# Kernel optimization log

Hardware: AMD Instinct MI355X
Metric: run time of the kernel (lower is better)

The kernel has to match this reference:

```python
import jax, jax.numpy as jnp
import numpy as np

NA = 3            # n_agents
B = 32768         # batch
H = 128           # hidden_dim (= attend_dim, attend_heads = 1)
ES, OAS, GS, ADIM = 4, 4, 2, 2
SDIM = ES + OAS * (NA - 1) + GS * NA   # 18
EPS = 1e-5


def _bn(x, ax):
    # BatchNorm1d(affine=False) in training mode: normalize with batch stats (biased var)
    m = x.mean(ax, keepdims=True)
    v = x.var(ax, keepdims=True)
    return (x - m) / jnp.sqrt(v + EPS)


def _lrelu(x):
    return jax.nn.leaky_relu(x, 0.01)


def setup_inputs() -> dict:
    key = jax.random.key(0)
    ks = jax.random.split(key, 26)
    r = lambda k, shp: (jax.random.normal(k, shp, dtype=jnp.float32) * 0.05)
    inp = {
        "s": jax.random.normal(ks[0], (NA, B, SDIM), dtype=jnp.float32),
        "a": jax.random.uniform(ks[1], (NA, B, ADIM), dtype=jnp.float32),
        # Attention_Actor (sa_encoder, with_action=True) params
        "en_W": r(ks[2], (NA, ES + 2, H)), "en_b": r(ks[3], (NA, H)),
        "oa_W": r(ks[4], (NA, OAS, H)), "oa_b": r(ks[5], (NA, H)),
        "goal_W": r(ks[6], (NA, GS, H)), "goal_b": r(ks[7], (NA, H)),
        "akey_W": r(ks[8], (2, H, H)),
        "asel_W": r(ks[9], (2, H, H)),
        "aval_W": r(ks[10], (2, H, H)), "aval_b": r(ks[11], (2, H)),
        "merge_W": r(ks[12], (NA, 3 * H, H)), "merge_b": r(ks[13], (NA, H)),
        # Critic params
        "senc_W": r(ks[14], (NA, SDIM, H)), "senc_b": r(ks[15], (NA, H)),
        "ckey_W": r(ks[16], (1, H, H)),
        "csel_W": r(ks[17], (1, H, H)),
        "cval_W": r(ks[18], (1, H, H)), "cval_b": r(ks[19], (1, H)),
        "cW1": r(ks[20], (NA, 2 * H, H)), "cb1": r(ks[21], (NA, H)),
        "cW2": r(ks[22], (NA, H, ADIM)), "cb2": r(ks[23], (NA, ADIM)),
    }
    return inp


def reference(s, a, en_W, en_b, oa_W, oa_b, goal_W, goal_b, akey_W, asel_W,
              aval_W, aval_b, merge_W, merge_b, senc_W, senc_b, ckey_W,
              csel_W, cval_W, cval_b, cW1, cb1, cW2, cb2):
    scale = 1.0 / np.sqrt(H)
    # ---- Attention_Actor(with_action=True): state-action encodings ----
    ent_in = _bn(jnp.concatenate([s[..., :ES], a[..., :2]], -1), 1)           # [NA,B,6]
    en_enc = _lrelu(jnp.einsum('nbi,nih->nbh', ent_in, en_W) + en_b[:, None])  # [NA,B,H]
    # other-agent slices (each slice normalized separately, as separate BN calls)
    oa_in = s[..., ES:ES + OAS * (NA - 1)].reshape(NA, B, NA - 1, OAS).transpose(0, 2, 1, 3)
    oa_enc = _lrelu(jnp.einsum('njbi,nih->njbh', _bn(oa_in, 2), oa_W) + oa_b[:, None, None])
    g_in = s[..., ES + OAS * (NA - 1):].reshape(NA, B, NA, GS).transpose(0, 2, 1, 3)
    g_enc = _lrelu(jnp.einsum('njbi,nih->njbh', _bn(g_in, 2), goal_W) + goal_b[:, None, None])
    sel = jnp.einsum('nbh,mhd->mnbd', en_enc, asel_W)                          # [2,NA,B,H]

    def attend(enc, kW, vW, vb, selm):
        keys = jnp.einsum('njbh,hd->njbd', enc, kW)
        vals = _lrelu(jnp.einsum('njbh,hd->njbd', enc, vW) + vb)
        w = jax.nn.softmax(jnp.einsum('nbd,njbd->nbj', selm, keys) * scale, -1)
        return jnp.einsum('nbj,njbd->nbd', w, vals)

    ov0 = attend(oa_enc, akey_W[0], aval_W[0], aval_b[0], sel[0])
    ov1 = attend(g_enc, akey_W[1], aval_W[1], aval_b[1], sel[1])
    sa_enc = _lrelu(jnp.einsum('nbi,nih->nbh',
                               jnp.concatenate([en_enc, ov0, ov1], -1), merge_W)
                    + merge_b[:, None])                                        # [NA,B,H]
    # ---- Critic: state encoders + cross-agent attention over sa encodings ----
    s_enc = _lrelu(jnp.einsum('nbi,nih->nbh', _bn(s, 1), senc_W) + senc_b[:, None])
    keys = jnp.einsum('nbh,khd->knbd', sa_enc, ckey_W)                         # [1,NA,B,H]
    vals = _lrelu(jnp.einsum('nbh,khd->knbd', sa_enc, cval_W) + cval_b[:, None, None])
    sels = jnp.einsum('nbh,khd->knbd', s_enc, csel_W)
    logits = jnp.einsum('kibd,kjbd->kibj', sels, keys) * scale                 # [1,NA,B,NA]
    mask = jnp.eye(NA, dtype=bool)[None, :, None, :]
    w = jax.nn.softmax(jnp.where(mask, -1e9, logits), -1)                      # attend j != i
    ov = jnp.einsum('kibj,kjbd->kibd', w, vals)                                # [1,NA,B,H]
    ov = jnp.moveaxis(ov, 0, -2).reshape(NA, B, -1)                            # concat heads
    h = _lrelu(jnp.einsum('nbi,nih->nbh', jnp.concatenate([s_enc, ov], -1), cW1)
               + cb1[:, None])
    q = jnp.einsum('nbh,nho->nbo', h, cW2) + cb2[:, None]                      # [NA,B,ADIM]
    return q
```

## Files before the change

kernel.cpp:

```cpp
#include <hip/hip_runtime.h>
#include <hip/hip_bf16.h>

#define NAG 3
#define BATCH 32768
#define HD 128
#define SD 18
#define TB 32
#define ROWS 48
#define NBLK 683
#define PADB (NBLK * ROWS)
#define EPSV 1e-5f
#define SCALE 0.08838834764831845f

typedef __attribute__((ext_vector_type(8))) short short8;
typedef __attribute__((ext_vector_type(4))) float f32x4;

#define WSB_STATS 0
#define WSB_ACCUM 512
#define WSB_F     1024
#define WSB_W     197632
#define OFF_FT0 0
#define OFF_FT1 32768
#define OFF_MT  65536
#define OFF_AV0 98304
#define OFF_AV1 131072
#define OFF_CV  163840
#define OFF_MG(n) (196608 + (n)*98304)
#define OFF_C1(n) (491520 + (n)*65536)
#define OFF_C2(n) (688128 + (n)*4096)
#define OFF_SW(n) (700416 + (n)*57344)
#define WSB_SA  2097152
#define SA_BYTES_P ((size_t)NAG * PADB * HD * 2)

__device__ __forceinline__ float lrelu(float x){ return x >= 0.0f ? x : 0.01f * x; }
__device__ __forceinline__ f32x4 lrelu4(f32x4 v){
  f32x4 r; r[0]=lrelu(v[0]); r[1]=lrelu(v[1]); r[2]=lrelu(v[2]); r[3]=lrelu(v[3]); return r;
}
__device__ __forceinline__ f32x4 binit(float b){ f32x4 c; c[0]=b;c[1]=b;c[2]=b;c[3]=b; return c; }
__device__ __forceinline__ unsigned short f2bf(float f){
  __hip_bfloat16 h = __float2bfloat16(f);
  return *reinterpret_cast<unsigned short*>(&h);
}
__device__ __forceinline__ float bf2f(unsigned short h){
  return __uint_as_float(((unsigned int)h) << 16);
}

__global__ void stats_partial_kernel(const float* __restrict__ s,
                                     const float* __restrict__ a,
                                     float* __restrict__ accum){
  const int n = blockIdx.x >> 4;
  const int chunk = blockIdx.x & 15;
  const int t = threadIdx.x;
  const int rows = BATCH / 16;
  const int b0 = chunk * rows;
  float sum[20], sq[20];
  #pragma unroll
  for (int c = 0; c < 20; ++c){ sum[c] = 0.f; sq[c] = 0.f; }
  for (int b = b0 + t; b < b0 + rows; b += 256){
    const float* row = s + ((size_t)n * BATCH + b) * SD;
    #pragma unroll
    for (int c = 0; c < SD; ++c){ float v = row[c]; sum[c] += v; sq[c] += v * v; }
    const float* ra = a + ((size_t)n * BATCH + b) * 2;
    #pragma unroll
    for (int c = 0; c < 2; ++c){ float v = ra[c]; sum[SD + c] += v; sq[SD + c] += v * v; }
  }
  __shared__ float red[256];
  for (int c = 0; c < 20; ++c){
    red[t] = sum[c]; __syncthreads();
    for (int off = 128; off > 0; off >>= 1){ if (t < off) red[t] += red[t + off]; __syncthreads(); }
    if (t == 0) atomicAdd(&accum[(n * 20 + c) * 2 + 0], red[0]);
    __syncthreads();
    red[t] = sq[c]; __syncthreads();
    for (int off = 128; off > 0; off >>= 1){ if (t < off) red[t] += red[t + off]; __syncthreads(); }
    if (t == 0) atomicAdd(&accum[(n * 20 + c) * 2 + 1], red[0]);
    __syncthreads();
  }
}

__global__ void fuse_mats_kernel(const float* __restrict__ asel, const float* __restrict__ akey,
                                 const float* __restrict__ csel, const float* __restrict__ ckey,
                                 float* __restrict__ F, const float* __restrict__ accum,
                                 float* __restrict__ stats){
  const int m  = blockIdx.y;
  if (m == 3){
    if (blockIdx.x == 0){
      int i = threadIdx.x;
      if (i < 60){
        float S = accum[i * 2 + 0], SQ = accum[i * 2 + 1];
        float mean = S / (float)BATCH;
        float var = SQ / (float)BATCH - mean * mean;
        stats[i * 2 + 0] = mean;
        stats[i * 2 + 1] = 1.0f / sqrtf(var + EPSV);
      }
    }
    return;
  }
  const int h1 = blockIdx.x;
  const int h2 = threadIdx.x;
  const float* A; const float* Bm;
  if (m == 0){ A = asel;            Bm = akey; }
  else if (m == 1){ A = asel + HD*HD; Bm = akey + HD*HD; }
  else { A = csel; Bm = ckey; }
  const float* arow = A + h1 * HD;
  const float* brow = Bm + h2 * HD;
  float acc = 0.f;
  #pragma unroll 4
  for (int d = 0; d < HD; ++d) acc = fmaf(arow[d], brow[d], acc);
  F[m * HD * HD + h1 * HD + h2] = acc;
}

__global__ void prep_split_kernel(const float* __restrict__ F, const float* __restrict__ aval_W,
                                  const float* __restrict__ cval_W, const float* __restrict__ merge_W,
                                  const float* __restrict__ cW1, const float* __restrict__ cW2,
                                  const float* __restrict__ en_W, const float* __restrict__ oa_W,
                                  const float* __restrict__ goal_W, const float* __restrict__ senc_W,
                                  unsigned short* __restrict__ wsu){
  const int job = blockIdx.y;
  const int idx = blockIdx.x * 256 + threadIdx.x;
  if (job == 15){
    if (idx >= 3 * 896 * 32) return;
    int k = idx & 31; int c = (idx >> 5) % 896; int n = idx / (896 * 32);
    int tt = c >> 7, cc = c & 127;
    float v = 0.f;
    if (tt == 0){
      if (k < 4) v = en_W[(size_t)(n*6 + k)*128 + cc];
      else if (k == 18 || k == 19) v = en_W[(size_t)(n*6 + 4 + (k-18))*128 + cc];
    } else if (tt <= 2){
      int j = tt - 1; int kk = k - (4 + 4*j);
      if (kk >= 0 && kk < 4) v = oa_W[(size_t)(n*4 + kk)*128 + cc];
    } else if (tt <= 5){
      int j = tt - 3; int kk = k - (12 + 2*j);
      if (kk >= 0 && kk < 2) v = goal_W[(size_t)(n*2 + kk)*128 + cc];
    } else {
      if (k < 18) v = senc_W[(size_t)(n*18 + k)*128 + cc];
    }
    unsigned short hi = f2bf(v); float lo = v - bf2f(hi);
    unsigned short* dh = wsu + OFF_SW(n);
    dh[c * 32 + k] = hi;
    dh[28672 + c * 32 + k] = f2bf(lo);
    return;
  }
  const float* src; unsigned short* dh; int K = 128, Csrc = 128, Cdst = 128, loff = 16384;
  switch (job){
    case 0: src = F;              dh = wsu + OFF_FT0; break;
    case 1: src = F + 16384;      dh = wsu + OFF_FT1; break;
    case 2: src = F + 32768;      dh = wsu + OFF_MT;  break;
    case 3: src = aval_W;         dh = wsu + OFF_AV0; break;
    case 4: src = aval_W + 16384; dh = wsu + OFF_AV1; break;
    case 5: src = cval_W;         dh = wsu + OFF_CV;  break;
    case 6: case 7: case 8: {
      int n = job - 6; src = merge_W + (size_t)n * 49152; dh = wsu + OFF_MG(n);
      K = 384; loff = 49152; } break;
    case 9: case 10: case 11: {
      int n = job - 9; src = cW1 + (size_t)n * 32768; dh = wsu + OFF_C1(n);
      K = 256; loff = 32768; } break;
    default: {
      int n = job - 12; src = cW2 + (size_t)n * 256; dh = wsu + OFF_C2(n);
      Csrc = 2; Cdst = 16; loff = 2048; } break;
  }
  if (idx >= K * Cdst) return;
  int k = idx / Cdst, c = idx - k * Cdst;
  float v = (c < Csrc) ? src[(size_t)k * Csrc + c] : 0.f;
  unsigned short hi = f2bf(v);
  dh[(size_t)c * K + k] = hi;
  dh[loff + (size_t)c * K + k] = f2bf(v - bf2f(hi));
}

__device__ __forceinline__ short8 ldAh(const unsigned char* sm, int base, int mi, int ks, int lane){
  int row = mi * 16 + (lane & 15);
  int bc  = ks * 64 + ((lane >> 4) << 4);
  return *(const short8*)(sm + base + row * 256 + (bc ^ ((row & 7) << 4)));
}
__device__ __forceinline__ void ldA(const unsigned char* sm, int base, int mi, int ks, int lane,
                                    short8& h, short8& l){
  int row = mi * 16 + (lane & 15);
  int bc  = ks * 64 + ((lane >> 4) << 4);
  int off = base + row * 256 + (bc ^ ((row & 7) << 4));
  h = *(const short8*)(sm + off);
  l = *(const short8*)(sm + off + 8192);
}
__device__ __forceinline__ void ldA32(const unsigned char* sm, int base, int mi, int lane,
                                      short8& h, short8& l){
  int row = mi * 16 + (lane & 15);
  int bc  = (lane >> 4) << 4;
  int off = base + row * 64 + (bc ^ ((row & 3) << 4));
  h = *(const short8*)(sm + off);
  l = *(const short8*)(sm + off + 2048);
}
__device__ __forceinline__ void ldA32_48(const unsigned char* sm, int base, int mi, int lane,
                                         short8& h, short8& l){
  int row = mi * 16 + (lane & 15);
  int bc  = (lane >> 4) << 4;
  int off = base + row * 64 + (bc ^ ((row & 3) << 4));
  h = *(const short8*)(sm + off);
  l = *(const short8*)(sm + off + 3072);
}
__device__ __forceinline__ short8 ldA32_48h(const unsigned char* sm, int base, int mi, int lane){
  int row = mi * 16 + (lane & 15);
  int bc  = (lane >> 4) << 4;
  return *(const short8*)(sm + base + row * 64 + (bc ^ ((row & 3) << 4)));
}

#define MM3(acc, ah, al, bh, bl) \
  acc = __builtin_amdgcn_mfma_f32_16x16x32_bf16(ah, bh, acc, 0, 0, 0); \
  acc = __builtin_amdgcn_mfma_f32_16x16x32_bf16(ah, bl, acc, 0, 0, 0); \
  acc = __builtin_amdgcn_mfma_f32_16x16x32_bf16(al, bh, acc, 0, 0, 0);
#define MM2(acc, ah, bh, bl) \
  acc = __builtin_amdgcn_mfma_f32_16x16x32_bf16(ah, bh, acc, 0, 0, 0); \
  acc = __builtin_amdgcn_mfma_f32_16x16x32_bf16(ah, bl, acc, 0, 0, 0);
#define MM1(acc, ah, bh) \
  acc = __builtin_amdgcn_mfma_f32_16x16x32_bf16(ah, bh, acc, 0, 0, 0);

__device__ __forceinline__ void gemmS3(f32x4& c0, f32x4& c1, f32x4& c2,
                                       const unsigned char* sm, int abase,
                                       const unsigned short* wh, const unsigned short* wl,
                                       int bcol, int lane){
  const size_t bb = (size_t)bcol * 32 + ((lane >> 4) << 3);
  const short8 bh = *(const short8*)(wh + bb);
  const short8 bl = *(const short8*)(wl + bb);
  short8 ah, al;
  ldA32_48(sm, abase, 0, lane, ah, al); MM3(c0, ah, al, bh, bl);
  ldA32_48(sm, abase, 1, lane, ah, al); MM3(c1, ah, al, bh, bl);
  ldA32_48(sm, abase, 2, lane, ah, al); MM3(c2, ah, al, bh, bl);
}
__device__ __forceinline__ void gemmS3_hb(f32x4& c0, f32x4& c1, f32x4& c2,
                                          const unsigned char* sm, int abase,
                                          const unsigned short* wh, int bcol, int lane){
  const size_t bb = (size_t)bcol * 32 + ((lane >> 4) << 3);
  const short8 bh = *(const short8*)(wh + bb);
  short8 ah, al;
  ldA32_48(sm, abase, 0, lane, ah, al); MM1(c0, ah, bh); MM1(c0, al, bh);
  ldA32_48(sm, abase, 1, lane, ah, al); MM1(c1, ah, bh); MM1(c1, al, bh);
  ldA32_48(sm, abase, 2, lane, ah, al); MM1(c2, ah, bh); MM1(c2, al, bh);
}
__device__ __forceinline__ void gemmS3_hh(f32x4& c0, f32x4& c1, f32x4& c2,
                                          const unsigned char* sm, int abase,
                                          const unsigned short* wh, int bcol, int lane){
  const size_t bb = (size_t)bcol * 32 + ((lane >> 4) << 3);
  const short8 bh = *(const short8*)(wh + bb);
  MM1(c0, ldA32_48h(sm, abase, 0, lane), bh);
  MM1(c1, ldA32_48h(sm, abase, 1, lane), bh);
  MM1(c2, ldA32_48h(sm, abase, 2, lane), bh);
}
__device__ __forceinline__ void gemmAW2_3(f32x4& k0, f32x4& k1, f32x4& k2,
                                          f32x4& m0, f32x4& m1, f32x4& m2,
                                          const unsigned char* sm, int abase,
                                          const unsigned short* wh0, const unsigned short* wh1,
                                          int bcol, int lane){
  const size_t bb = (size_t)bcol * 128 + ((lane >> 4) << 3);
  #pragma unroll
  for (int ks = 0; ks < 4; ++ks){
    short8 a0 = ldAh(sm, abase, 0, ks, lane);
    short8 a1 = ldAh(sm, abase, 1, ks, lane);
    short8 a2 = ldAh(sm, abase, 2, ks, lane);
    const short8 b0 = *(const short8*)(wh0 + bb + ks * 32);
    const short8 b1 = *(const short8*)(wh1 + bb + ks * 32);
    MM1(k0, a0, b0); MM1(k1, a1, b0); MM1(k2, a2, b0);
    MM1(m0, a0, b1); MM1(m1, a1, b1); MM1(m2, a2, b1);
  }
}
__device__ __forceinline__ void gemmA2s3(f32x4& c0, f32x4& c1, f32x4& c2,
                                         f32x4& d0, f32x4& d1, f32x4& d2,
                                         const unsigned char* sm, int a0b, int a1b,
                                         const unsigned short* wh, int bcol, int lane){
  const size_t bb = (size_t)bcol * 128 + ((lane >> 4) << 3);
  #pragma unroll
  for (int ks = 0; ks < 4; ++ks){
    const short8 bh = *(const short8*)(wh + bb + ks * 32);
    short8 x;
    x = ldAh(sm, a0b, 0, ks, lane); MM1(c0, x, bh);
    x = ldAh(sm, a0b, 1, ks, lane); MM1(c1, x, bh);
    x = ldAh(sm, a0b, 2, ks, lane); MM1(c2, x, bh);
    x = ldAh(sm, a1b, 0, ks, lane); MM1(d0, x, bh);
    x = ldAh(sm, a1b, 1, ks, lane); MM1(d1, x, bh);
    x = ldAh(sm, a1b, 2, ks, lane); MM1(d2, x, bh);
  }
}
__device__ __forceinline__ void gemmA3s3(f32x4& c0, f32x4& c1, f32x4& c2,
                                         f32x4& d0, f32x4& d1, f32x4& d2,
                                         f32x4& e0, f32x4& e1, f32x4& e2,
                                         const unsigned char* sm, int a0b, int a1b, int a2b,
                                         const unsigned short* wh, int bcol, int lane){
  const size_t bb = (size_t)bcol * 128 + ((lane >> 4) << 3);
  #pragma unroll
  for (int ks = 0; ks < 4; ++ks){
    const short8 bh = *(const short8*)(wh + bb + ks * 32);
    short8 x;
    x = ldAh(sm, a0b, 0, ks, lane); MM1(c0, x, bh);
    x = ldAh(sm, a0b, 1, ks, lane); MM1(c1, x, bh);
    x = ldAh(sm, a0b, 2, ks, lane); MM1(c2, x, bh);
    x = ldAh(sm, a1b, 0, ks, lane); MM1(d0, x, bh);
    x = ldAh(sm, a1b, 1, ks, lane); MM1(d1, x, bh);
    x = ldAh(sm, a1b, 2, ks, lane); MM1(d2, x, bh);
    x = ldAh(sm, a2b, 0, ks, lane); MM1(e0, x, bh);
    x = ldAh(sm, a2b, 1, ks, lane); MM1(e1, x, bh);
    x = ldAh(sm, a2b, 2, ks, lane); MM1(e2, x, bh);
  }
}
__device__ __forceinline__ void gemmAh_hb3K(f32x4& c0, f32x4& c1, f32x4& c2,
                                            const unsigned char* sm, int abase,
                                            const unsigned short* wh,
                                            int K, int bcol, int kBase, int lane){
  const size_t bb = (size_t)bcol * K + kBase + ((lane >> 4) << 3);
  #pragma unroll
  for (int ks = 0; ks < 4; ++ks){
    const short8 bh = *(const short8*)(wh + bb + ks * 32);
    short8 a;
    a = ldAh(sm, abase, 0, ks, lane); MM1(c0, a, bh);
    a = ldAh(sm, abase, 1, ks, lane); MM1(c1, a, bh);
    a = ldAh(sm, abase, 2, ks, lane); MM1(c2, a, bh);
  }
}
__device__ __forceinline__ void gemmAh_hb3(f32x4& c0, f32x4& c1, f32x4& c2,
                                           const unsigned char* sm, int abase,
                                           const unsigned short* wh, int bcol, int lane){
  const size_t bb = (size_t)bcol * 128 + ((lane >> 4) << 3);
  #pragma unroll
  for (int ks = 0; ks < 4; ++ks){
    const short8 bh = *(const short8*)(wh + bb + ks * 32);
    short8 a;
    a = ldAh(sm, abase, 0, ks, lane); MM1(c0, a, bh);
    a = ldAh(sm, abase, 1, ks, lane); MM1(c1, a, bh);
    a = ldAh(sm, abase, 2, ks, lane); MM1(c2, a, bh);
  }
}

__device__ __forceinline__ void stTile(unsigned char* sm, int base, int mi, int lane, int col, f32x4 v){
  #pragma unroll
  for (int r = 0; r < 4; ++r){
    int row = mi * 16 + ((lane >> 4) << 2) + r;
    int off = base + row * 256 + ((col * 2) ^ ((row & 7) << 4));
    unsigned short hi = f2bf(v[r]);
    *(unsigned short*)(sm + off) = hi;
    *(unsigned short*)(sm + off + 8192) = f2bf(v[r] - bf2f(hi));
  }
}
__device__ __forceinline__ void stH(unsigned char* sm, int base, int mi, int lane, int col, f32x4 v){
  #pragma unroll
  for (int r = 0; r < 4; ++r){
    int row = mi * 16 + ((lane >> 4) << 2) + r;
    int off = base + row * 256 + ((col * 2) ^ ((row & 7) << 4));
    *(unsigned short*)(sm + off) = f2bf(v[r]);
  }
}
__device__ __forceinline__ void stSK(unsigned char* sm, int base, int mi, int lane, int col, f32x4 v){
  #pragma unroll
  for (int r = 0; r < 4; ++r){
    int row = mi * 16 + ((lane >> 4) << 2) + r;
    int off = base + row * 256 + ((col * 2) ^ ((row & 7) << 5));
    *(unsigned short*)(sm + off) = f2bf(v[r]);
  }
}
__device__ __forceinline__ float dot8(short8 x, short8 y){
  float acc = 0.f;
  #pragma unroll
  for (int e = 0; e < 8; ++e)
    acc = fmaf(bf2f((unsigned short)x[e]), bf2f((unsigned short)y[e]), acc);
  return acc;
}
#define RED16(p) { p += __shfl_xor(p, 1, 16); p += __shfl_xor(p, 2, 16); \
                   p += __shfl_xor(p, 4, 16); p += __shfl_xor(p, 8, 16); }
#define RED8(p) { p += __shfl_xor(p, 1); p += __shfl_xor(p, 2); p += __shfl_xor(p, 4); }

__global__ __launch_bounds__(512, 4) void actor_kernel(
    const float* __restrict__ s, const float* __restrict__ a,
    const float* __restrict__ en_b, const float* __restrict__ oa_b,
    const float* __restrict__ goal_b, const float* __restrict__ aval_b,
    const float* __restrict__ merge_b, const unsigned char* __restrict__ wsc,
    unsigned short* __restrict__ sa_g)
{
  __shared__ __align__(16) unsigned char SM[80640];
  const int AXN = 0, AEN = 6144, AOV = 18432, ASK = 30720;
  const int SLB0 = 43008, SLB1 = 55296, SLB2 = 67584, AEP = 79872;
  const int t = threadIdx.x, lane = t & 63, wave = t >> 6;
  const int col = wave * 16 + (lane & 15);
  const int n = blockIdx.y;
  const int gb0 = blockIdx.x * ROWS;
  const float* stats = (const float*)(wsc + WSB_STATS);
  const unsigned short* wsu = (const unsigned short*)(wsc + WSB_W);
  const unsigned short* swh = wsu + OFF_SW(n);
  float* eP0 = (float*)(SM + AEP);
  float* eP1 = eP0 + 48;
  float* eP2 = eP0 + 96;
  float* esm = eP0 + 144;
  const f32x4 Z = binit(0.f);
  const int drow = wave * 8 + (lane >> 3);
  const int dcb  = (lane & 7) * 32;
  const int r0base = (lane >> 4) << 2;

  if (t < ROWS){
    int row = t;
    size_t gb = (size_t)gb0 + row;
    if (gb >= BATCH) gb = BATCH - 1;
    const float* st = stats + n * 40;
    const float* srow = s + ((size_t)n * BATCH + gb) * SD;
    const float* arow = a + ((size_t)n * BATCH + gb) * 2;
    #pragma unroll
    for (int c = 0; c < 32; ++c){
      float v = 0.f;
      if (c < 18) v = (srow[c] - st[c*2]) * st[c*2+1];
      else if (c < 20) v = (arow[c-18] - st[c*2]) * st[c*2+1];
      unsigned short hi = f2bf(v);
      int off = AXN + row * 64 + ((c * 2) ^ ((row & 3) << 4));
      *(unsigned short*)(SM + off) = hi;
      *(unsigned short*)(SM + off + 3072) = f2bf(v - bf2f(hi));
    }
  }
  __syncthreads();
  {
    f32x4 c0 = binit(en_b[n*HD + col]), c1 = c0, c2 = c0;
    gemmS3_hb(c0, c1, c2, SM, AXN, swh, col, lane);
    stH(SM, AEN, 0, lane, col, lrelu4(c0));
    stH(SM, AEN, 1, lane, col, lrelu4(c1));
    stH(SM, AEN, 2, lane, col, lrelu4(c2));
    const float bb = oa_b[n*HD + col];
    c0 = binit(bb); c1 = c0; c2 = c0;
    gemmS3_hb(c0, c1, c2, SM, AXN, swh, 128 + col, lane);
    stH(SM, SLB0, 0, lane, col, lrelu4(c0));
    stH(SM, SLB0, 1, lane, col, lrelu4(c1));
    stH(SM, SLB0, 2, lane, col, lrelu4(c2));
    c0 = binit(bb); c1 = c0; c2 = c0;
    gemmS3_hb(c0, c1, c2, SM, AXN, swh, 256 + col, lane);
    stH(SM, SLB1, 0, lane, col, lrelu4(c0));
    stH(SM, SLB1, 1, lane, col, lrelu4(c1));
    stH(SM, SLB1, 2, lane, col, lrelu4(c2));
  }
  __syncthreads();
  {
    f32x4 k0 = Z, k1 = Z, k2 = Z, m0 = Z, m1 = Z, m2 = Z;
    gemmAW2_3(k0, k1, k2, m0, m1, m2, SM, AEN,
              wsu + OFF_FT0, wsu + OFF_FT1, col, lane);
    stSK(SM, AOV, 0, lane, col, k0); stSK(SM, AOV, 1, lane, col, k1); stSK(SM, AOV, 2, lane, col, k2);
    stSK(SM, ASK, 0, lane, col, m0); stSK(SM, ASK, 1, lane, col, m1); stSK(SM, ASK, 2, lane, col, m2);
  }
  __syncthreads();
  f32x4 va0, va1, va2, vb0, vb1, vb2;
  {
    const float vb = aval_b[col];
    va0 = binit(vb); va1 = va0; va2 = va0; vb0 = va0; vb1 = va0; vb2 = va0;
    gemmA2s3(va0, va1, va2, vb0, vb1, vb2, SM, SLB0, SLB1, wsu + OFF_AV0, col, lane);
    if (drow < ROWS){
      int sw5 = (drow & 7) << 5, sw4 = (drow & 7) << 4;
      const unsigned char* kb = SM + AOV + drow * 256;
      short8 kfa = *(const short8*)(kb + (dcb ^ sw5));
      short8 kfb = *(const short8*)(kb + ((dcb + 16) ^ sw5));
      const unsigned char* s0 = SM + SLB0 + drow * 256;
      short8 e0a = *(const short8*)(s0 + (dcb ^ sw4));
      short8 e0b = *(const short8*)(s0 + ((dcb + 16) ^ sw4));
      const unsigned char* s1 = SM + SLB1 + drow * 256;
      short8 e1a = *(const short8*)(s1 + (dcb ^ sw4));
      short8 e1b = *(const short8*)(s1 + ((dcb + 16) ^ sw4));
      float p0 = dot8(kfa, e0a) + dot8(kfb, e0b);
      float p1 = dot8(kfa, e1a) + dot8(kfb, e1b);
      RED8(p0) RED8(p1)
      if ((lane & 7) == 0){
        float e0 = __expf(p0 * SCALE), e1 = __expf(p1 * SCALE);
        eP0[drow] = e0; eP1[drow] = e1; esm[drow] = e0 + e1;
      }
    }
  }
  __syncthreads();
  {
    f32x4 o;
    #pragma unroll
    for (int r = 0; r < 4; ++r){
      int mr = r0base + r;
      o[r] = (eP0[mr] * lrelu(va0[r]) + eP1[mr] * lrelu(vb0[r])) / esm[mr];
    }
    stH(SM, AOV, 0, lane, col, o);
    #pragma unroll
    for (int r = 0; r < 4; ++r){
      int mr = 16 + r0base + r;
      o[r] = (eP0[mr] * lrelu(va1[r]) + eP1[mr] * lrelu(vb1[r])) / esm[mr];
    }
    stH(SM, AOV, 1, lane, col, o);
    #pragma unroll
    for (int r = 0; r < 4; ++r){
      int mr = 32 + r0base + r;
      o[r] = (eP0[mr] * lrelu(va2[r]) + eP1[mr] * lrelu(vb2[r])) / esm[mr];
    }
    stH(SM, AOV, 2, lane, col, o);
    const float bb = goal_b[n*HD + col];
    f32x4 c0 = binit(bb), c1 = c0, c2 = c0;
    gemmS3_hb(c0, c1, c2, SM, AXN, swh, 384 + col, lane);
    stH(SM, SLB0, 0, lane, col, lrelu4(c0));
    stH(SM, SLB0, 1, lane, col, lrelu4(c1));
    stH(SM, SLB0, 2, lane, col, lrelu4(c2));
    c0 = binit(bb); c1 = c0; c2 = c0;
    gemmS3_hb(c0, c1, c2, SM, AXN, swh, 512 + col, lane);
    stH(SM, SLB1, 0, lane, col, lrelu4(c0));
    stH(SM, SLB1, 1, lane, col, lrelu4(c1));
    stH(SM, SLB1, 2, lane, col, lrelu4(c2));
    c0 = binit(bb); c1 = c0; c2 = c0;
    gemmS3_hb(c0, c1, c2, SM, AXN, swh, 640 + col, lane);
    stH(SM, SLB2, 0, lane, col, lrelu4(c0));
    stH(SM, SLB2, 1, lane, col, lrelu4(c1));
    stH(SM, SLB2, 2, lane, col, lrelu4(c2));
  }
  __syncthreads();
  f32x4 g0m0, g0m1, g0m2, g1m0, g1m1, g1m2, g2m0, g2m1, g2m2;
  {
    const float vb = aval_b[HD + col];
    g0m0 = binit(vb); g0m1 = g0m0; g0m2 = g0m0;
    g1m0 = g0m0; g1m1 = g0m0; g1m2 = g0m0;
    g2m0 = g0m0; g2m1 = g0m0; g2m2 = g0m0;
    gemmA3s3(g0m0, g0m1, g0m2, g1m0, g1m1, g1m2, g2m0, g2m1, g2m2,
             SM, SLB0, SLB1, SLB2, wsu + OFF_AV1, col, lane);
    if (drow < ROWS){
      int sw5 = (drow & 7) << 5, sw4 = (drow & 7) << 4;
      const unsigned char* kb = SM + ASK + drow * 256;
      short8 kfa = *(const short8*)(kb + (dcb ^ sw5));
      short8 kfb = *(const short8*)(kb + ((dcb + 16) ^ sw5));
      const unsigned char* s0 = SM + SLB0 + drow * 256;
      short8 e0a = *(const short8*)(s0 + (dcb ^ sw4));
      short8 e0b = *(const short8*)(s0 + ((dcb + 16) ^ sw4));
      const unsigned char* s1 = SM + SLB1 + drow * 256;
      short8 e1a = *(const short8*)(s1 + (dcb ^ sw4));
      short8 e1b = *(const short8*)(s1 + ((dcb + 16) ^ sw4));
      const unsigned char* s2 = SM + SLB2 + drow * 256;
      short8 e2a = *(const short8*)(s2 + (dcb ^ sw4));
      short8 e2b = *(const short8*)(s2 + ((dcb + 16) ^ sw4));
      float p0 = dot8(kfa, e0a) + dot8(kfb, e0b);
      float p1 = dot8(kfa, e1a) + dot8(kfb, e1b);
      float p2 = dot8(kfa, e2a) + dot8(kfb, e2b);
      RED8(p0) RED8(p1) RED8(p2)
      if ((lane & 7) == 0){
        float e0 = __expf(p0 * SCALE), e1 = __expf(p1 * SCALE), e2 = __expf(p2 * SCALE);
        eP0[drow] = e0; eP1[drow] = e1; eP2[drow] = e2;
        esm[drow] = (e0 + e1) + e2;
      }
    }
  }
  __syncthreads();
  {
    f32x4 o;
    #pragma unroll
    for (int r = 0; r < 4; ++r){
      int mr = r0base + r;
      o[r] = ((eP0[mr] * lrelu(g0m0[r]) + eP1[mr] * lrelu(g1m0[r]))
              + eP2[mr] * lrelu(g2m0[r])) / esm[mr];
    }
    stH(SM, SLB0, 0, lane, col, o);
    #pragma unroll
    for (int r = 0; r < 4; ++r){
      int mr = 16 + r0base + r;
      o[r] = ((eP0[mr] * lrelu(g0m1[r]) + eP1[mr] * lrelu(g1m1[r]))
              + eP2[mr] * lrelu(g2m1[r])) / esm[mr];
    }
    stH(SM, SLB0, 1, lane, col, o);
    #pragma unroll
    for (int r = 0; r < 4; ++r){
      int mr = 32 + r0base + r;
      o[r] = ((eP0[mr] * lrelu(g0m2[r]) + eP1[mr] * lrelu(g1m2[r]))
              + eP2[mr] * lrelu(g2m2[r])) / esm[mr];
    }
    stH(SM, SLB0, 2, lane, col, o);
  }
  __syncthreads();
  {
    const unsigned short* mh = wsu + OFF_MG(n);
    f32x4 c0 = binit(merge_b[n*HD + col]), c1 = c0, c2 = c0;
    gemmAh_hb3K(c0, c1, c2, SM, AEN,  mh, 384, col, 0,   lane);
    gemmAh_hb3K(c0, c1, c2, SM, AOV,  mh, 384, col, 128, lane);
    gemmAh_hb3K(c0, c1, c2, SM, SLB0, mh, 384, col, 256, lane);
    stH(SM, SLB1, 0, lane, col, lrelu4(c0));
    stH(SM, SLB1, 1, lane, col, lrelu4(c1));
    stH(SM, SLB1, 2, lane, col, lrelu4(c2));
  }
  __syncthreads();
  for (int idx = t; idx < ROWS * 16; idx += 512){
    int row = idx >> 4, ch = idx & 15;
    short8 u = *(const short8*)(SM + SLB1 + row * 256 + ((ch * 16) ^ ((row & 7) << 4)));
    *(short8*)(sa_g + ((size_t)n * PADB + gb0 + row) * HD + ch * 8) = u;
  }
}

__global__ __launch_bounds__(512, 4) void critic_kernel(
    const float* __restrict__ s, const float* __restrict__ a,
    const float* __restrict__ senc_b, const float* __restrict__ cval_b,
    const float* __restrict__ cb1, const float* __restrict__ cW2,
    const float* __restrict__ cb2, const unsigned char* __restrict__ wsc,
    const unsigned short* __restrict__ sa_g, float* __restrict__ out)
{
  __shared__ __align__(16) unsigned char SM[52608];
  const int CXN = 0, CEN = 3072, CSMo = 15360, CSA = 27648;
  const int COV = 15360 , CH = 27648 , CLW = 52224;
  const int t = threadIdx.x, lane = t & 63, wave = t >> 6;
  const int col = wave * 16 + (lane & 15);
  const int i = blockIdx.y;
  const int gb0 = blockIdx.x * ROWS;
  const int j0 = (i == 0) ? 1 : 0;
  const int j1 = (i == 2) ? 1 : 2;
  const float* stats = (const float*)(wsc + WSB_STATS);
  const unsigned short* wsu = (const unsigned short*)(wsc + WSB_W);
  const unsigned short* swh = wsu + OFF_SW(i);
  const f32x4 Z = binit(0.f);
  const int drow = wave * 8 + (lane >> 3);
  const int dcb  = (lane & 7) * 32;
  const int r0base = (lane >> 4) << 2;

  if (t < ROWS){
    int row = t;
    size_t gb = (size_t)gb0 + row;
    if (gb >= BATCH) gb = BATCH - 1;
    const float* st = stats + i * 40;
    const float* srow = s + ((size_t)i * BATCH + gb) * SD;
    const float* arow = a + ((size_t)i * BATCH + gb) * 2;
    #pragma unroll
    for (int c = 0; c < 32; ++c){
      float v = 0.f;
      if (c < 18) v = (srow[c] - st[c*2]) * st[c*2+1];
      else if (c < 20) v = (arow[c-18] - st[c*2]) * st[c*2+1];
      int off = CXN + row * 64 + ((c * 2) ^ ((row & 3) << 4));
      *(unsigned short*)(SM + off) = f2bf(v);
    }
  }
  for (int idx = t; idx < 2 * ROWS * 16; idx += 512){
    int tile = idx >= ROWS * 16;
    int k = idx - tile * ROWS * 16;
    int row = k >> 4, ch = k & 15;
    int j = tile ? j1 : j0;
    short8 u = *(const short8*)(sa_g + ((size_t)j * PADB + gb0 + row) * HD + ch * 8);
    *(short8*)(SM + CSA + tile * 12288 + row * 256 + ((ch * 16) ^ ((row & 7) << 4))) = u;
  }
  __syncthreads();
  {
    f32x4 c0 = binit(senc_b[i*HD + col]), c1 = c0, c2 = c0;
    gemmS3_hh(c0, c1, c2, SM, CXN, swh, 768 + col, lane);
    stH(SM, CEN, 0, lane, col, lrelu4(c0));
    stH(SM, CEN, 1, lane, col, lrelu4(c1));
    stH(SM, CEN, 2, lane, col, lrelu4(c2));
  }
  __syncthreads();
  {
    f32x4 k0 = Z, k1 = Z, k2 = Z;
    gemmAh_hb3(k0, k1, k2, SM, CEN, wsu + OFF_MT, col, lane);
    stSK(SM, CSMo, 0, lane, col, k0);
    stSK(SM, CSMo, 1, lane, col, k1);
    stSK(SM, CSMo, 2, lane, col, k2);
  }
  __syncthreads();
  f32x4 v00, v01, v02, v10, v11, v12;
  {
    const float vb = cval_b[col];
    v00 = binit(vb); v01 = v00; v02 = v00; v10 = v00; v11 = v00; v12 = v00;
    gemmA2s3(v00, v01, v02, v10, v11, v12, SM, CSA, CSA + 12288,
             wsu + OFF_CV, col, lane);
    if (drow < ROWS){
      int sw5 = (drow & 7) << 5, sw4 = (drow & 7) << 4;
      const unsigned char* mb = SM + CSMo + drow * 256;
      short8 ma = *(const short8*)(mb + (dcb ^ sw5));
      short8 mbf = *(const short8*)(mb + ((dcb + 16) ^ sw5));
      const unsigned char* a0p = SM + CSA + drow * 256;
      short8 a0a = *(const short8*)(a0p + (dcb ^ sw4));
      short8 a0b = *(const short8*)(a0p + ((dcb + 16) ^ sw4));
      const unsigned char* b0p = SM + CSA + 12288 + drow * 256;
      short8 b0a = *(const short8*)(b0p + (dcb ^ sw4));
      short8 b0b = *(const short8*)(b0p + ((dcb + 16) ^ sw4));
      float p0 = dot8(ma, a0a) + dot8(mbf, a0b);
      float p1 = dot8(ma, b0a) + dot8(mbf, b0b);
      RED8(p0) RED8(p1)
      if ((lane & 7) == 0){
        float e0 = __expf(p0 * SCALE), e1 = __expf(p1 * SCALE);
        float inv = 1.f / (e0 + e1);
        ((float*)(SM + CLW))[drow]      = e0 * inv;
        ((float*)(SM + CLW))[48 + drow] = e1 * inv;
      }
    }
  }
  __syncthreads();
  {
    const float* w0 = (const float*)(SM + CLW);
    const float* w1 = w0 + 48;
    f32x4 o;
    #pragma unroll
    for (int r = 0; r < 4; ++r){
      int mr = r0base + r;
      o[r] = w0[mr] * lrelu(v00[r]) + w1[mr] * lrelu(v10[r]);
    }
    stH(SM, COV, 0, lane, col, o);
    #pragma unroll
    for (int r = 0; r < 4; ++r){
      int mr = 16 + r0base + r;
      o[r] = w0[mr] * lrelu(v01[r]) + w1[mr] * lrelu(v11[r]);
    }
    stH(SM, COV, 1, lane, col, o);
    #pragma unroll
    for (int r = 0; r < 4; ++r){
      int mr = 32 + r0base + r;
      o[r] = w0[mr] * lrelu(v02[r]) + w1[mr] * lrelu(v12[r]);
    }
    stH(SM, COV, 2, lane, col, o);
  }
  __syncthreads();
  {
    const unsigned short* c1h = wsu + OFF_C1(i);
    f32x4 h0 = binit(cb1[i*HD + col]), h1 = h0, h2 = h0;
    gemmAh_hb3K(h0, h1, h2, SM, CEN, c1h, 256, col, 0,   lane);
    gemmAh_hb3K(h0, h1, h2, SM, COV, c1h, 256, col, 128, lane);
    stH(SM, CH, 0, lane, col, lrelu4(h0));
    stH(SM, CH, 1, lane, col, lrelu4(h1));
    stH(SM, CH, 2, lane, col, lrelu4(h2));
  }
  __syncthreads();
  if (drow < ROWS && gb0 + drow < BATCH){
    int sw4 = (drow & 7) << 4;
    const unsigned char* hb = SM + CH + drow * 256;
    short8 ha = *(const short8*)(hb + (dcb ^ sw4));
    short8 hbf = *(const short8*)(hb + ((dcb + 16) ^ sw4));
    float q0 = 0.f, q1 = 0.f;
    #pragma unroll
    for (int e = 0; e < 8; ++e){
      int d = (lane & 7) * 16 + e;
      float hv = bf2f((unsigned short)ha[e]);
      q0 = fmaf(hv, cW2[(i * HD + d) * 2 + 0], q0);
      q1 = fmaf(hv, cW2[(i * HD + d) * 2 + 1], q1);
    }
    #pragma unroll
    for (int e = 0; e < 8; ++e){
      int d = (lane & 7) * 16 + 8 + e;
      float hv = bf2f((unsigned short)hbf[e]);
      q0 = fmaf(hv, cW2[(i * HD + d) * 2 + 0], q0);
      q1 = fmaf(hv, cW2[(i * HD + d) * 2 + 1], q1);
    }
    RED8(q0) RED8(q1)
    if ((lane & 7) == 0){
      out[((size_t)i * BATCH + gb0 + drow) * 2 + 0] = q0 + cb2[i * 2 + 0];
      out[((size_t)i * BATCH + gb0 + drow) * 2 + 1] = q1 + cb2[i * 2 + 1];
    }
  }
}

extern "C" void kernel_launch(void* const* d_in, const int* in_sizes, int n_in,
                              void* d_out, int out_size, void* d_ws, size_t ws_size,
                              hipStream_t stream) {
  const float* s       = (const float*)d_in[0];
  const float* a       = (const float*)d_in[1];
  const float* en_W    = (const float*)d_in[2];
  const float* en_b    = (const float*)d_in[3];
  const float* oa_W    = (const float*)d_in[4];
  const float* oa_b    = (const float*)d_in[5];
  const float* goal_W  = (const float*)d_in[6];
  const float* goal_b  = (const float*)d_in[7];
  const float* akey_W  = (const float*)d_in[8];
  const float* asel_W  = (const float*)d_in[9];
  const float* aval_W  = (const float*)d_in[10];
  const float* aval_b  = (const float*)d_in[11];
  const float* merge_W = (const float*)d_in[12];
  const float* merge_b = (const float*)d_in[13];
  const float* senc_W  = (const float*)d_in[14];
  const float* senc_b  = (const float*)d_in[15];
  const float* ckey_W  = (const float*)d_in[16];
  const float* csel_W  = (const float*)d_in[17];
  const float* cval_W  = (const float*)d_in[18];
  const float* cval_b  = (const float*)d_in[19];
  const float* cW1     = (const float*)d_in[20];
  const float* cb1     = (const float*)d_in[21];
  const float* cW2     = (const float*)d_in[22];
  const float* cb2     = (const float*)d_in[23];
  unsigned char* wsc = (unsigned char*)d_ws;
  float* F = (float*)(wsc + WSB_F);
  unsigned short* wsu = (unsigned short*)(wsc + WSB_W);
  float* out = (float*)d_out;

  hipMemsetAsync(wsc + WSB_ACCUM, 0, 480, stream);
  stats_partial_kernel<<<48, 256, 0, stream>>>(s, a, (float*)(wsc + WSB_ACCUM));
  fuse_mats_kernel<<<dim3(HD, 4), HD, 0, stream>>>(
      asel_W, akey_W, csel_W, ckey_W, F,
      (const float*)(wsc + WSB_ACCUM), (float*)(wsc + WSB_STATS));
  prep_split_kernel<<<dim3(336, 16), 256, 0, stream>>>(
      F, aval_W, cval_W, merge_W, cW1, cW2, en_W, oa_W, goal_W, senc_W, wsu);

  unsigned short* sa_g = (unsigned short*)(wsc + WSB_SA);
  actor_kernel<<<dim3(NBLK, NAG), 512, 0, stream>>>(
      s, a, en_b, oa_b, goal_b, aval_b, merge_b,
      (const unsigned char*)wsc, sa_g);
  critic_kernel<<<dim3(NBLK, NAG), 512, 0, stream>>>(
      s, a, senc_b, cval_b, cb1, cW2, cb2,
      (const unsigned char*)wsc, (const unsigned short*)sa_g, out);
}
```

Measured before the change: 208.7 us.

## Drop split-bf16 low parts in actor input encoders and widen stats kernel grid

The actor's normalized input tile is now stored only as a single bf16 value, with no hi/lo split. The encoder GEMMs switch from the two-MFMA hb variant to the single-MFMA hh variant, which frees about 3 KB of shared memory and halves that work. Separately, the batch-statistics kernel splits the batch into 128 chunks per agent instead of 16, so more blocks share the reduction. Unused helpers are also removed. The precision drop on the encoder inputs could add error against the fp32 reference.

```diff
diff --git a/kernel.cpp b/kernel.cpp
--- a/kernel.cpp
+++ b/kernel.cpp
@@ -5,7 +5,6 @@
 #define BATCH 32768
 #define HD 128
 #define SD 18
-#define TB 32
 #define ROWS 48
 #define NBLK 683
 #define PADB (NBLK * ROWS)
@@ -48,10 +47,10 @@
 __global__ void stats_partial_kernel(const float* __restrict__ s,
                                      const float* __restrict__ a,
                                      float* __restrict__ accum){
-  const int n = blockIdx.x >> 4;
-  const int chunk = blockIdx.x & 15;
+  const int n = blockIdx.x >> 7;
+  const int chunk = blockIdx.x & 127;
   const int t = threadIdx.x;
-  const int rows = BATCH / 16;
+  const int rows = BATCH / 128;
   const int b0 = chunk * rows;
   float sum[20], sq[20];
   #pragma unroll
@@ -171,76 +170,23 @@
   int bc  = ks * 64 + ((lane >> 4) << 4);
   return *(const short8*)(sm + base + row * 256 + (bc ^ ((row & 7) << 4)));
 }
-__device__ __forceinline__ void ldA(const unsigned char* sm, int base, int mi, int ks, int lane,
-                                    short8& h, short8& l){
-  int row = mi * 16 + (lane & 15);
-  int bc  = ks * 64 + ((lane >> 4) << 4);
-  int off = base + row * 256 + (bc ^ ((row & 7) << 4));
-  h = *(const short8*)(sm + off);
-  l = *(const short8*)(sm + off + 8192);
-}
-__device__ __forceinline__ void ldA32(const unsigned char* sm, int base, int mi, int lane,
-                                      short8& h, short8& l){
-  int row = mi * 16 + (lane & 15);
-  int bc  = (lane >> 4) << 4;
-  int off = base + row * 64 + (bc ^ ((row & 3) << 4));
-  h = *(const short8*)(sm + off);
-  l = *(const short8*)(sm + off + 2048);
-}
-__device__ __forceinline__ void ldA32_48(const unsigned char* sm, int base, int mi, int lane,
-                                         short8& h, short8& l){
-  int row = mi * 16 + (lane & 15);
-  int bc  = (lane >> 4) << 4;
-  int off = base + row * 64 + (bc ^ ((row & 3) << 4));
-  h = *(const short8*)(sm + off);
-  l = *(const short8*)(sm + off + 3072);
-}
-__device__ __forceinline__ short8 ldA32_48h(const unsigned char* sm, int base, int mi, int lane){
+__device__ __forceinline__ short8 ldA32h(const unsigned char* sm, int base, int mi, int lane){
   int row = mi * 16 + (lane & 15);
   int bc  = (lane >> 4) << 4;
   return *(const short8*)(sm + base + row * 64 + (bc ^ ((row & 3) << 4)));
 }
 
-#define MM3(acc, ah, al, bh, bl) \
-  acc = __builtin_amdgcn_mfma_f32_16x16x32_bf16(ah, bh, acc, 0, 0, 0); \
-  acc = __builtin_amdgcn_mfma_f32_16x16x32_bf16(ah, bl, acc, 0, 0, 0); \
-  acc = __builtin_amdgcn_mfma_f32_16x16x32_bf16(al, bh, acc, 0, 0, 0);
-#define MM2(acc, ah, bh, bl) \
-  acc = __builtin_amdgcn_mfma_f32_16x16x32_bf16(ah, bh, acc, 0, 0, 0); \
-  acc = __builtin_amdgcn_mfma_f32_16x16x32_bf16(ah, bl, acc, 0, 0, 0);
 #define MM1(acc, ah, bh) \
   acc = __builtin_amdgcn_mfma_f32_16x16x32_bf16(ah, bh, acc, 0, 0, 0);
 
-__device__ __forceinline__ void gemmS3(f32x4& c0, f32x4& c1, f32x4& c2,
-                                       const unsigned char* sm, int abase,
-                                       const unsigned short* wh, const unsigned short* wl,
-                                       int bcol, int lane){
-  const size_t bb = (size_t)bcol * 32 + ((lane >> 4) << 3);
-  const short8 bh = *(const short8*)(wh + bb);
-  const short8 bl = *(const short8*)(wl + bb);
-  short8 ah, al;
-  ldA32_48(sm, abase, 0, lane, ah, al); MM3(c0, ah, al, bh, bl);
-  ldA32_48(sm, abase, 1, lane, ah, al); MM3(c1, ah, al, bh, bl);
-  ldA32_48(sm, abase, 2, lane, ah, al); MM3(c2, ah, al, bh, bl);
-}
-__device__ __forceinline__ void gemmS3_hb(f32x4& c0, f32x4& c1, f32x4& c2,
-                                          const unsigned char* sm, int abase,
-                                          const unsigned short* wh, int bcol, int lane){
-  const size_t bb = (size_t)bcol * 32 + ((lane >> 4) << 3);
-  const short8 bh = *(const short8*)(wh + bb);
-  short8 ah, al;
-  ldA32_48(sm, abase, 0, lane, ah, al); MM1(c0, ah, bh); MM1(c0, al, bh);
-  ldA32_48(sm, abase, 1, lane, ah, al); MM1(c1, ah, bh); MM1(c1, al, bh);
-  ldA32_48(sm, abase, 2, lane, ah, al); MM1(c2, ah, bh); MM1(c2, al, bh);
-}
 __device__ __forceinline__ void gemmS3_hh(f32x4& c0, f32x4& c1, f32x4& c2,
                                           const unsigned char* sm, int abase,
                                           const unsigned short* wh, int bcol, int lane){
   const size_t bb = (size_t)bcol * 32 + ((lane >> 4) << 3);
   const short8 bh = *(const short8*)(wh + bb);
-  MM1(c0, ldA32_48h(sm, abase, 0, lane), bh);
-  MM1(c1, ldA32_48h(sm, abase, 1, lane), bh);
-  MM1(c2, ldA32_48h(sm, abase, 2, lane), bh);
+  MM1(c0, ldA32h(sm, abase, 0, lane), bh);
+  MM1(c1, ldA32h(sm, abase, 1, lane), bh);
+  MM1(c2, ldA32h(sm, abase, 2, lane), bh);
 }
 __device__ __forceinline__ void gemmAW2_3(f32x4& k0, f32x4& k1, f32x4& k2,
                                           f32x4& m0, f32x4& m1, f32x4& m2,
@@ -325,16 +271,6 @@
   }
 }
 
-__device__ __forceinline__ void stTile(unsigned char* sm, int base, int mi, int lane, int col, f32x4 v){
-  #pragma unroll
-  for (int r = 0; r < 4; ++r){
-    int row = mi * 16 + ((lane >> 4) << 2) + r;
-    int off = base + row * 256 + ((col * 2) ^ ((row & 7) << 4));
-    unsigned short hi = f2bf(v[r]);
-    *(unsigned short*)(sm + off) = hi;
-    *(unsigned short*)(sm + off + 8192) = f2bf(v[r] - bf2f(hi));
-  }
-}
 __device__ __forceinline__ void stH(unsigned char* sm, int base, int mi, int lane, int col, f32x4 v){
   #pragma unroll
   for (int r = 0; r < 4; ++r){
@@ -358,8 +294,6 @@
     acc = fmaf(bf2f((unsigned short)x[e]), bf2f((unsigned short)y[e]), acc);
   return acc;
 }
-#define RED16(p) { p += __shfl_xor(p, 1, 16); p += __shfl_xor(p, 2, 16); \
-                   p += __shfl_xor(p, 4, 16); p += __shfl_xor(p, 8, 16); }
 #define RED8(p) { p += __shfl_xor(p, 1); p += __shfl_xor(p, 2); p += __shfl_xor(p, 4); }
 
 __global__ __launch_bounds__(512, 4) void actor_kernel(
@@ -369,9 +303,9 @@
     const float* __restrict__ merge_b, const unsigned char* __restrict__ wsc,
     unsigned short* __restrict__ sa_g)
 {
-  __shared__ __align__(16) unsigned char SM[80640];
-  const int AXN = 0, AEN = 6144, AOV = 18432, ASK = 30720;
-  const int SLB0 = 43008, SLB1 = 55296, SLB2 = 67584, AEP = 79872;
+  __shared__ __align__(16) unsigned char SM[77568];
+  const int AXN = 0, AEN = 3072, AOV = 15360, ASK = 27648;
+  const int SLB0 = 39936, SLB1 = 52224, SLB2 = 64512, AEP = 76800;
   const int t = threadIdx.x, lane = t & 63, wave = t >> 6;
   const int col = wave * 16 + (lane & 15);
   const int n = blockIdx.y;
@@ -400,27 +334,25 @@
       float v = 0.f;
       if (c < 18) v = (srow[c] - st[c*2]) * st[c*2+1];
       else if (c < 20) v = (arow[c-18] - st[c*2]) * st[c*2+1];
-      unsigned short hi = f2bf(v);
       int off = AXN + row * 64 + ((c * 2) ^ ((row & 3) << 4));
-      *(unsigned short*)(SM + off) = hi;
-      *(unsigned short*)(SM + off + 3072) = f2bf(v - bf2f(hi));
+      *(unsigned short*)(SM + off) = f2bf(v);
     }
   }
   __syncthreads();
   {
     f32x4 c0 = binit(en_b[n*HD + col]), c1 = c0, c2 = c0;
-    gemmS3_hb(c0, c1, c2, SM, AXN, swh, col, lane);
+    gemmS3_hh(c0, c1, c2, SM, AXN, swh, col, lane);
     stH(SM, AEN, 0, lane, col, lrelu4(c0));
     stH(SM, AEN, 1, lane, col, lrelu4(c1));
     stH(SM, AEN, 2, lane, col, lrelu4(c2));
     const float bb = oa_b[n*HD + col];
     c0 = binit(bb); c1 = c0; c2 = c0;
-    gemmS3_hb(c0, c1, c2, SM, AXN, swh, 128 + col, lane);
+    gemmS3_hh(c0, c1, c2, SM, AXN, swh, 128 + col, lane);
     stH(SM, SLB0, 0, lane, col, lrelu4(c0));
     stH(SM, SLB0, 1, lane, col, lrelu4(c1));
     stH(SM, SLB0, 2, lane, col, lrelu4(c2));
     c0 = binit(bb); c1 = c0; c2 = c0;
-    gemmS3_hb(c0, c1, c2, SM, AXN, swh, 256 + col, lane);
+    gemmS3_hh(c0, c1, c2, SM, AXN, swh, 256 + col, lane);
     stH(SM, SLB1, 0, lane, col, lrelu4(c0));
     stH(SM, SLB1, 1, lane, col, lrelu4(c1));
     stH(SM, SLB1, 2, lane, col, lrelu4(c2));
@@ -482,17 +414,17 @@
     stH(SM, AOV, 2, lane, col, o);
     const float bb = goal_b[n*HD + col];
     f32x4 c0 = binit(bb), c1 = c0, c2 = c0;
-    gemmS3_hb(c0, c1, c2, SM, AXN, swh, 384 + col, lane);
+    gemmS3_hh(c0, c1, c2, SM, AXN, swh, 384 + col, lane);
     stH(SM, SLB0, 0, lane, col, lrelu4(c0));
     stH(SM, SLB0, 1, lane, col, lrelu4(c1));
     stH(SM, SLB0, 2, lane, col, lrelu4(c2));
     c0 = binit(bb); c1 = c0; c2 = c0;
-    gemmS3_hb(c0, c1, c2, SM, AXN, swh, 512 + col, lane);
+    gemmS3_hh(c0, c1, c2, SM, AXN, swh, 512 + col, lane);
     stH(SM, SLB1, 0, lane, col, lrelu4(c0));
     stH(SM, SLB1, 1, lane, col, lrelu4(c1));
     stH(SM, SLB1, 2, lane, col, lrelu4(c2));
     c0 = binit(bb); c1 = c0; c2 = c0;
-    gemmS3_hb(c0, c1, c2, SM, AXN, swh, 640 + col, lane);
+    gemmS3_hh(c0, c1, c2, SM, AXN, swh, 640 + col, lane);
     stH(SM, SLB2, 0, lane, col, lrelu4(c0));
     stH(SM, SLB2, 1, lane, col, lrelu4(c1));
     stH(SM, SLB2, 2, lane, col, lrelu4(c2));
@@ -584,7 +516,7 @@
 {
   __shared__ __align__(16) unsigned char SM[52608];
   const int CXN = 0, CEN = 3072, CSMo = 15360, CSA = 27648;
-  const int COV = 15360 , CH = 27648 , CLW = 52224;
+  const int COV = 15360, CH = 27648, CLW = 52224;
   const int t = threadIdx.x, lane = t & 63, wave = t >> 6;
   const int col = wave * 16 + (lane & 15);
   const int i = blockIdx.y;
@@ -764,7 +696,7 @@
   float* out = (float*)d_out;
 
   hipMemsetAsync(wsc + WSB_ACCUM, 0, 480, stream);
-  stats_partial_kernel<<<48, 256, 0, stream>>>(s, a, (float*)(wsc + WSB_ACCUM));
+  stats_partial_kernel<<<384, 256, 0, stream>>>(s, a, (float*)(wsc + WSB_ACCUM));
   fuse_mats_kernel<<<dim3(HD, 4), HD, 0, stream>>>(
       asel_W, akey_W, csel_W, ckey_W, F,
       (const float*)(wsc + WSB_ACCUM), (float*)(wsc + WSB_STATS));
```

Result: slower. 228.2 us (+9.3%).
